# Performance work log

Measured on AMD Instinct MI355X. Metric: run time of the kernel, lower is better.

The kernel has to match this reference:

```python
import jax, jax.numpy as jnp
import numpy as np

OBS, PRED = 8, 12
EIN, EHID, NOISE = 64, 256, 64
GEMB = 64
DHID = EHID + NOISE  # 320
G, NPER = 8, 192
B = G * NPER


def leaky(x):
    return jnp.where(x > 0, x, 0.2 * x)


def lstm_cell(x, h, c, Wih, Whh, bih, bhh):
    gates = x @ Wih.T + bih + h @ Whh.T + bhh
    i, f, g, o = jnp.split(gates, 4, axis=-1)
    c = jax.nn.sigmoid(f) * c + jax.nn.sigmoid(i) * jnp.tanh(g)
    h = jax.nn.sigmoid(o) * jnp.tanh(c)
    return h, c


def kmeans(x, k, niter=10):
    # deterministic init: first k points (torch used randperm)
    c = x[:k]
    ar = jnp.arange(k)
    for _ in range(niter):
        d2 = ((x[:, None, :] - c[None, :, :]) ** 2).sum(-1)  # [N,k]
        a = jnp.argmin(d2, axis=1)
        onehot = (a[:, None] == ar[None, :]).astype(x.dtype)  # [N,k]
        cnt = onehot.sum(0)
        mean = (onehot.T @ x) / jnp.maximum(cnt, 1.0)[:, None]
        c = jnp.where((cnt == 0)[:, None], x[:k], mean)  # reseed dead clusters
    d2 = ((x[:, None, :] - c[None, :, :]) ** 2).sum(-1)
    return jnp.argmin(d2, axis=1)


def signed_graph(node, W_ne, b_ne, W_att, b_att):
    n, D = node.shape
    emb = node @ W_ne.T + b_ne  # [n,E]
    E = emb.shape[1]
    a_other, a_self = W_att[0, :E], W_att[0, E:]
    # e[i,j] = a_other.emb[j] + a_self.emb[i] + b  (cat([other, self]) order)
    e = (emb @ a_other)[None, :] + (emb @ a_self)[:, None] + b_att[0]
    edge = jax.nn.softmax(leaky(e), axis=0)
    edge = jnp.triu(edge, 0) + jnp.triu(edge, 1).T  # symmetrize from upper tri
    d = edge.sum(1)
    L = jnp.diag(d) - edge
    dinv = 1.0 / jnp.sqrt(d)
    L_sym = dinv[:, None] * L * dinv[None, :]
    lam, H = jnp.linalg.eigh(jax.lax.stop_gradient(L_sym))  # ascending eigvals
    H = H[:, :2]  # two smallest
    Hn = H / jnp.sqrt((H ** 2).sum(1, keepdims=True))
    labels = kmeans(Hn, int(np.ceil(n / 2)))
    same = labels[:, None] == labels[None, :]
    NEG = jnp.float32(-1e8)
    pos_alpha = jax.nn.softmax(leaky(edge * jnp.where(same, 1.0, NEG)), axis=0)
    neg_alpha = jax.nn.softmax(leaky(edge * jnp.where(same, NEG, 1.0)), axis=0)
    feat = jax.nn.relu(pos_alpha[..., None] * node[None, :, :]) + \
           jax.nn.relu(neg_alpha[..., None] * node[None, :, :])  # [n,n,D]
    return feat.sum(axis=1)


def setup_inputs():
    key = jax.random.key(0)
    ks = jax.random.split(key, 22)
    p = lambda k, s: jax.random.normal(k, s, jnp.float32) * 0.1
    starts = jnp.arange(G, dtype=jnp.int32) * NPER
    return {
        "input_traj": jax.random.normal(ks[0], (OBS + PRED, B, 2), jnp.float32),
        "enc_h0": jax.random.normal(ks[1], (B, EHID), jnp.float32),
        "enc_c0": jax.random.normal(ks[2], (B, EHID), jnp.float32),
        "noise_z": jax.random.normal(ks[3], (G, NOISE), jnp.float32),
        "W_emb": p(ks[4], (EIN, 2)), "b_emb": p(ks[5], (EIN,)),
        "Wih_e": p(ks[6], (4 * EHID, EIN)), "Whh_e": p(ks[7], (4 * EHID, EHID)),
        "bih_e": p(ks[8], (4 * EHID,)), "bhh_e": p(ks[9], (4 * EHID,)),
        "Wih_d": p(ks[10], (4 * DHID, EIN)), "Whh_d": p(ks[11], (4 * DHID, DHID)),
        "bih_d": p(ks[12], (4 * DHID,)), "bhh_d": p(ks[13], (4 * DHID,)),
        "W_out": p(ks[14], (2, DHID)), "b_out": p(ks[15], (2,)),
        "W_ne": p(ks[16], (GEMB, DHID)), "b_ne": p(ks[17], (GEMB,)),
        "W_att": p(ks[18], (1, 2 * GEMB)), "b_att": p(ks[19], (1,)),
        "seq_start_end": jnp.stack([starts, starts + NPER], axis=1),
    }


def reference(input_traj, enc_h0, enc_c0, noise_z, W_emb, b_emb,
              Wih_e, Whh_e, bih_e, bhh_e, Wih_d, Whh_d, bih_d, bhh_d,
              W_out, b_out, W_ne, b_ne, W_att, b_att, seq_start_end):
    # ---- encoder ----
    x = jax.nn.relu(input_traj @ W_emb.T + b_emb)  # [T,B,EIN]
    def step(carry, xt):
        h, c = carry
        h, c = lstm_cell(xt, h, c, Wih_e, Whh_e, bih_e, bhh_e)
        return (h, c), None
    (h_enc, _), _ = jax.lax.scan(step, (enc_h0, enc_c0), x[:OBS])
    # ---- add per-scene noise (equal-sized scenes) ----
    z = jnp.repeat(noise_z, NPER, axis=0)  # [B,NOISE]
    h = jnp.concatenate([h_enc, z], axis=1)  # [B,DHID]
    c = jnp.zeros_like(h)
    traj_out = input_traj[OBS - 1]  # [B,2]
    sg = jax.vmap(lambda nd: signed_graph(nd, W_ne, b_ne, W_att, b_att))
    preds = []
    for i in range(PRED):  # eval mode: no teacher forcing
        inp = jax.nn.relu(traj_out @ W_emb.T + b_emb)
        if i % 12 == 4:
            h = sg(h.reshape(G, NPER, DHID)).reshape(B, DHID)
        h, c = lstm_cell(inp, h, c, Wih_d, Whh_d, bih_d, bhh_d)
        traj_out = h @ W_out.T + b_out
        preds.append(traj_out)
    return jnp.stack(preds)  # [PRED,B,2]
```

## Files before the change

### kernel.cpp

```cpp
#include <hip/hip_runtime.h>
#include <hip/hip_bf16.h>

typedef __hip_bfloat16 bf16;

#define NN 192
#define NG 8
#define BB 1536
#define EHID 256
#define DH 320
#define PRED 12
#define STRD 192
#define ATILE (NN*STRD)

__device__ __forceinline__ int aoffc(int r, int c){
  int c4 = c >> 2;
  int s = (c4 & ~7) | ((c4 + 3*r) & 7);
  return r*STRD + (s << 2) + (c & 3);
}

#define WAVE_SYNC() do { asm volatile("" ::: "memory"); __builtin_amdgcn_wave_barrier(); } while (0)

__device__ __forceinline__ float waveSum(float v){
#pragma unroll
  for (int o = 32; o > 0; o >>= 1) v += __shfl_down(v, o);
  return v;
}
__device__ __forceinline__ double waveSumD(double v){
#pragma unroll
  for (int o = 32; o > 0; o >>= 1) v += __shfl_down(v, o);
  return v;
}
__device__ __forceinline__ float waveAllSum(float v){
#pragma unroll
  for (int o = 32; o > 0; o >>= 1) v += __shfl_xor(v, o);
  return v;
}
__device__ __forceinline__ double waveAllSumD(double v){
#pragma unroll
  for (int o = 32; o > 0; o >>= 1) v += __shfl_xor(v, o);
  return v;
}

__device__ __forceinline__ double blockSumD(double v, double* red){
  int lane = threadIdx.x & 63, wid = threadIdx.x >> 6, nw = (int)blockDim.x >> 6;
  double s = waveSumD(v);
  __syncthreads();
  if (lane == 0) red[wid] = s;
  __syncthreads();
  if (wid == 0){
    double t = (lane < nw) ? red[lane] : 0.0;
    t = waveSumD(t);
    if (lane == 0) red[0] = t;
  }
  __syncthreads();
  return red[0];
}


__global__ void k_zero_int(int* __restrict__ p, int n){
  int i = blockIdx.x*blockDim.x + threadIdx.x;
  if (i < n) p[i] = 0;
}
__global__ void k_zero_f(float* __restrict__ p, int n){
  int i = blockIdx.x*blockDim.x + threadIdx.x;
  if (i < n) p[i] = 0.f;
}

__global__ void k_probe(const unsigned short* __restrict__ src, int n, int* __restrict__ cnt){
  int tid = blockIdx.x*blockDim.x + threadIdx.x;
  int stride = gridDim.x*blockDim.x;
  int bad = 0;
  for (int j = tid; j < n; j += stride){
    float v = __uint_as_float(((unsigned int)src[j]) << 16);
    if (!(fabsf(v) < 100.f)) bad++;
  }
#pragma unroll
  for (int o = 32; o > 0; o >>= 1) bad += __shfl_down(bad, o);
  if ((threadIdx.x & 63) == 0 && bad > 0) atomicAdd(cnt, bad);
}
__global__ void k_flag(const int* __restrict__ cnt, int* __restrict__ flag){
  *flag = (*cnt > 4096) ? 1 : 0;
}

struct CvtArgs {
  const void* src[20];
  float*      dst[20];
  int         n[20];
};

__global__ void k_convert(CvtArgs a, const int* __restrict__ flag){
  int id = blockIdx.y;
  int n = a.n[id];
  float* d = a.dst[id];
  int t = blockIdx.x*blockDim.x + threadIdx.x;
  int stride = gridDim.x*blockDim.x;
  if (*flag == 0){
    const bf16* s = (const bf16*)a.src[id];
    for (int j = t; j < n; j += stride) d[j] = __bfloat162float(s[j]);
  } else {
    const float* s = (const float*)a.src[id];
    for (int j = t; j < n; j += stride) d[j] = s[j];
  }
}


__global__ void k_embed(const float* __restrict__ in, const float* __restrict__ W,
                        const float* __restrict__ b, float* __restrict__ out){
  int r = blockIdx.x, e = threadIdx.x;
  float x = in[r*2], y = in[r*2+1];
  float v = W[e*2]*x + W[e*2+1]*y + b[e];
  out[r*64+e] = v > 0.f ? v : 0.f;
}

__global__ void k_concat(const float* __restrict__ henc, const float* __restrict__ z,
                         float* __restrict__ h){
  int idx = blockIdx.x*blockDim.x + threadIdx.x;
  if (idx >= BB*DH) return;
  int b = idx / DH, j = idx - b*DH;
  h[idx] = (j < EHID) ? henc[b*EHID + j] : z[(b/NN)*64 + (j - EHID)];
}

__global__ void k_copy_f(const float* __restrict__ in, float* __restrict__ dst, int n){
  int i = blockIdx.x*blockDim.x + threadIdx.x;
  if (i < n) dst[i] = in[i];
}

__global__ __launch_bounds__(256) void k_gates(
    const float* __restrict__ A1, const float* __restrict__ W1, int K1,
    const float* __restrict__ A2, const float* __restrict__ W2, int K2,
    const float* __restrict__ b1, const float* __restrict__ b2,
    float* __restrict__ C, int N){
  __shared__ __align__(16) float As[32][68];
  __shared__ __align__(16) float Ws[32][68];
  int tid = threadIdx.x;
  int tx = tid & 15, ty = tid >> 4;
  int n0 = blockIdx.x * 64, m0 = blockIdx.y * 64;
  float acc[4][4] = {};
  for (int ph = 0; ph < 2; ++ph){
    const float* A = ph ? A2 : A1;
    const float* W = ph ? W2 : W1;
    int K = ph ? K2 : K1;
    for (int k0 = 0; k0 < K; k0 += 32){
      {
        int am = tid >> 2, ak = (tid & 3) * 8;
        const float* srcA = A + (size_t)(m0+am)*K + k0 + ak;
        float4 f0 = *(const float4*)(srcA);
        float4 f1 = *(const float4*)(srcA+4);
        As[ak+0][am]=f0.x; As[ak+1][am]=f0.y; As[ak+2][am]=f0.z; As[ak+3][am]=f0.w;
        As[ak+4][am]=f1.x; As[ak+5][am]=f1.y; As[ak+6][am]=f1.z; As[ak+7][am]=f1.w;
        const float* srcW = W + (size_t)(n0+am)*K + k0 + ak;
        float4 w0 = *(const float4*)(srcW);
        float4 w1 = *(const float4*)(srcW+4);
        Ws[ak+0][am]=w0.x; Ws[ak+1][am]=w0.y; Ws[ak+2][am]=w0.z; Ws[ak+3][am]=w0.w;
        Ws[ak+4][am]=w1.x; Ws[ak+5][am]=w1.y; Ws[ak+6][am]=w1.z; Ws[ak+7][am]=w1.w;
      }
      __syncthreads();
#pragma unroll
      for (int k = 0; k < 32; ++k){
        float4 a0 = *(const float4*)&As[k][ty*4];
        float4 b0 = *(const float4*)&Ws[k][tx*4];
        float av[4] = {a0.x, a0.y, a0.z, a0.w};
        float bv[4] = {b0.x, b0.y, b0.z, b0.w};
#pragma unroll
        for (int i = 0; i < 4; ++i)
#pragma unroll
          for (int j = 0; j < 4; ++j)
            acc[i][j] += av[i]*bv[j];
      }
      __syncthreads();
    }
  }
  float bs[4];
#pragma unroll
  for (int j = 0; j < 4; ++j){
    int col = n0 + tx*4 + j;
    bs[j] = b1[col] + b2[col];
  }
#pragma unroll
  for (int i = 0; i < 4; ++i){
    int row = m0 + ty*4 + i;
    float4 v;
    v.x = acc[i][0] + bs[0]; v.y = acc[i][1] + bs[1];
    v.z = acc[i][2] + bs[2]; v.w = acc[i][3] + bs[3];
    *(float4*)&C[(size_t)row*N + n0 + tx*4] = v;
  }
}

__global__ void k_lstm(const float* __restrict__ gates, float* __restrict__ c,
                       float* __restrict__ h, int H){
  int idx = blockIdx.x*blockDim.x + threadIdx.x;
  if (idx >= BB*H) return;
  int b = idx / H, j = idx - b*H;
  const float* g = gates + (size_t)b*4*H;
  float gi = g[j], gf = g[H+j], gg = g[2*H+j], go = g[3*H+j];
  float si = 1.f/(1.f+expf(-gi));
  float sf = 1.f/(1.f+expf(-gf));
  float so = 1.f/(1.f+expf(-go));
  float cc = sf*c[idx] + si*tanhf(gg);
  c[idx] = cc;
  h[idx] = so*tanhf(cc);
}

__global__ void k_outproj(const float* __restrict__ h, const float* __restrict__ W,
                          const float* __restrict__ bo, float* __restrict__ traj,
                          void* __restrict__ outbase, int step, const int* __restrict__ flag){
  int b = blockIdx.x, lane = threadIdx.x;
  const float* hb = h + (size_t)b*DH;
  float a0 = 0.f, a1 = 0.f;
  for (int k = lane; k < DH; k += 64){
    float hv = hb[k];
    a0 += hv*W[k];
    a1 += hv*W[DH+k];
  }
  a0 = waveSum(a0); a1 = waveSum(a1);
  if (lane == 0){
    a0 += bo[0]; a1 += bo[1];
    traj[b*2] = a0; traj[b*2+1] = a1;
    size_t idx = (size_t)step*BB*2 + (size_t)b*2;
    if (*flag == 0){
      bf16* o = (bf16*)outbase;
      o[idx] = __float2bfloat16(a0); o[idx+1] = __float2bfloat16(a1);
    } else {
      float* o = (float*)outbase;
      o[idx] = a0; o[idx+1] = a1;
    }
  }
}


__global__ void k_sg_emb(const float* __restrict__ h, const float* __restrict__ Wne,
                         const float* __restrict__ bne, const float* __restrict__ Watt,
                         double* __restrict__ sself, double* __restrict__ sother){
  int node = blockIdx.x, e = threadIdx.x;
  const float* hb = h + (size_t)node*DH;
  double acc = (double)bne[e];
  for (int k = 0; k < DH; ++k) acc += (double)hb[k]*(double)Wne[e*DH+k];
  double po = acc * (double)Watt[e];
  double ps = acc * (double)Watt[64+e];
  po = waveSumD(po); ps = waveSumD(ps);
  if (e == 0){ sother[node] = po; sself[node] = ps; }
}

__global__ void k_sg_edgecol(const double* __restrict__ sself, const double* __restrict__ sother,
                             const float* __restrict__ batt, double* __restrict__ edge){
  int g = blockIdx.x, j = threadIdx.x;
  const double* ss = sself + g*NN;
  double bb = (double)batt[0];
  double sj = sother[g*NN + j];
  double m = -1e300;
  for (int i = 0; i < NN; ++i){
    double e = ss[i] + sj + bb; e = e > 0.0 ? e : 0.2*e;
    m = fmax(m, e);
  }
  double sum = 0.0;
  for (int i = 0; i < NN; ++i){
    double e = ss[i] + sj + bb; e = e > 0.0 ? e : 0.2*e;
    sum += exp(e - m);
  }
  double* E = edge + (size_t)g*NN*NN;
  for (int i = 0; i < NN; ++i){
    double e = ss[i] + sj + bb; e = e > 0.0 ? e : 0.2*e;
    E[i*NN + j] = exp(e - m)/sum;
  }
}

__global__ void k_sg_sym(const double* __restrict__ edge, double* __restrict__ esym){
  int idx = blockIdx.x*blockDim.x + threadIdx.x;
  if (idx >= NG*NN*NN) return;
  int g = idx / (NN*NN), r = idx - g*NN*NN;
  int i = r / NN, j = r - i*NN;
  const double* E = edge + (size_t)g*NN*NN;
  esym[idx] = (i <= j) ? E[i*NN + j] : E[j*NN + i];
}

__global__ void k_sg_dsum(const double* __restrict__ esym, double* __restrict__ darr){
  int i = blockIdx.x*blockDim.x + threadIdx.x;
  if (i >= NG*NN) return;
  int g = i / NN, li = i - g*NN;
  const double* E = esym + (size_t)g*NN*NN + (size_t)li*NN;
  double s = 0.0;
  for (int j = 0; j < NN; ++j) s += E[j];
  darr[i] = fmax(s, 1e-300);
}

__global__ void k_sg_lsym(const double* __restrict__ esym, const double* __restrict__ darr,
                          float* __restrict__ Afull){
  int idx = blockIdx.x*blockDim.x + threadIdx.x;
  if (idx >= NG*NN*NN) return;
  int g = idx / (NN*NN), r = idx - g*NN*NN;
  int i = r / NN, j = r - i*NN;
  double w = esym[idx];
  double lij = (i == j) ? (darr[g*NN+i] - w) : (-w);
  Afull[(size_t)g*ATILE + aoffc(i, j)] =
      (float)(lij / (sqrt(darr[g*NN+i])*sqrt(darr[g*NN+j])));
}

__global__ __launch_bounds__(256) void k_sg_eigen(const float* __restrict__ Afull,
                                                   const double* __restrict__ darr,
                                                   double* __restrict__ v1out){
  extern __shared__ unsigned char ldsraw[];
  float*  A     = (float*)ldsraw;
  double* dd    = (double*)(ldsraw + 147456);
  double* ee    = dd + NN;
  double* yv    = ee + NN;
  double* lu_d  = yv + NN;
  double* lu_du = lu_d + NN;
  double* lu_du2= lu_du + NN;
  double* redA  = lu_du2 + NN;
  double* redB  = redA + 16;
  double* salpha= redB + 16;
  float*  uu    = (float*)(ldsraw + 156944);
  float*  ww    = uu + NN;
  int*    lu_piv= (int*)(ww + NN);
  double* lu_dl = (double*)uu;

  int g = blockIdx.x, tid = threadIdx.x;
  int lane = tid & 63, wid = tid >> 6;

  const float* src = Afull + (size_t)g*ATILE;
  for (int t = tid*4; t < ATILE; t += 1024) *(float4*)&A[t] = *(const float4*)&src[t];
  __syncthreads();

  for (int k = 0; k < NN-65; ++k){
    int m = NN-1-k;
    int i = k+1+tid;
    float x = 0.f;
    if (tid < m) x = A[aoffc(i, k)];
    if (tid == 0) *salpha = (double)x;
    float part = (tid > 0 && tid < m) ? x*x : 0.f;
    part = waveSum(part);
    if (lane == 0) redA[wid] = (double)part;
    __syncthreads();
    double sigma = redA[0] + redA[1] + redA[2] + redA[3];
    double alpha = *salpha;
    double beta, tau, scale;
    if (sigma <= 1e-30){ tau = 0.0; beta = alpha; scale = 0.0; }
    else {
      beta = -copysign(sqrt(alpha*alpha + sigma), alpha);
      tau = (beta - alpha)/beta;
      scale = 1.0/(alpha - beta);
    }
    float tau_f = (float)tau, scale_f = (float)scale;
    if (tid == 0){
      dd[k] = (double)A[aoffc(k, k)];
      ee[k] = beta;
      A[aoffc(k, k)] = tau_f;
    }
    if (tau != 0.0){
      float u_i = 0.f;
      if (tid < m){
        u_i = (tid == 0) ? 1.f : x*scale_f;
        uu[i] = u_i;
        if (tid >= 1) A[aoffc(i, k)] = u_i;
      }
      __syncthreads();
      float p = 0.f;
      if (tid < m){
        const int rb = i*STRD;
        const int rk3 = (3*i) & 7;
        int off[8];
#pragma unroll
        for (int j = 0; j < 8; ++j) off[j] = ((j + rk3) & 7) << 2;
        float s0=0.f, s1=0.f, s2=0.f, s3=0.f, accs=0.f;
        int c = k+1;
        int cA = (c+3)&~3, cB = (c+31)&~31;
        for (; c < cA; ++c) accs += A[aoffc(i, c)]*uu[c];
        for (; c < cB; c += 4){
          int c4 = c>>2; int s = (c4&~7)|((c4+rk3)&7);
          float4 a4 = *(const float4*)&A[rb + (s<<2)];
          float4 u4 = *(const float4*)&uu[c];
          s0 += a4.x*u4.x; s1 += a4.y*u4.y; s2 += a4.z*u4.z; s3 += a4.w*u4.w;
        }
        for (; c < NN; c += 32){
          const int cb = rb + c;
#pragma unroll
          for (int j = 0; j < 8; ++j){
            float4 a4 = *(const float4*)&A[cb + off[j]];
            float4 u4 = *(const float4*)&uu[c + 4*j];
            s0 += a4.x*u4.x; s1 += a4.y*u4.y; s2 += a4.z*u4.z; s3 += a4.w*u4.w;
          }
        }
        p = tau_f * (((s0+s1)+(s2+s3)) + accs);
      }
      float vp = u_i*p;
      vp = waveSum(vp);
      if (lane == 0) redB[wid] = (double)vp;
      __syncthreads();
      double vtp = redB[0] + redB[1] + redB[2] + redB[3];
      float Kc_f = (float)(0.5*tau*vtp);
      float w_i = 0.f;
      if (tid < m){
        w_i = p - Kc_f*u_i;
        ww[i] = w_i;
      }
      __syncthreads();
      if (tid < m){
        const int rb = i*STRD;
        const int rk3 = (3*i) & 7;
        int off[8];
#pragma unroll
        for (int j = 0; j < 8; ++j) off[j] = ((j + rk3) & 7) << 2;
        int c = k+1;
        int cA = (c+3)&~3, cB = (c+31)&~31;
        for (; c < cA; ++c) A[aoffc(i, c)] -= u_i*ww[c] + w_i*uu[c];
        for (; c < cB; c += 4){
          int c4 = c>>2; int s = (c4&~7)|((c4+rk3)&7);
          float* ap = &A[rb + (s<<2)];
          float4 a4 = *(const float4*)ap;
          float4 u4 = *(const float4*)&uu[c];
          float4 w4 = *(const float4*)&ww[c];
          a4.x -= u_i*w4.x + w_i*u4.x;
          a4.y -= u_i*w4.y + w_i*u4.y;
          a4.z -= u_i*w4.z + w_i*u4.z;
          a4.w -= u_i*w4.w + w_i*u4.w;
          *(float4*)ap = a4;
        }
        for (; c < NN; c += 32){
          const int cb = rb + c;
#pragma unroll
          for (int j = 0; j < 8; ++j){
            float* ap = &A[cb + off[j]];
            float4 a4 = *(const float4*)ap;
            float4 u4 = *(const float4*)&uu[c + 4*j];
            float4 w4 = *(const float4*)&ww[c + 4*j];
            a4.x -= u_i*w4.x + w_i*u4.x;
            a4.y -= u_i*w4.y + w_i*u4.y;
            a4.z -= u_i*w4.z + w_i*u4.z;
            a4.w -= u_i*w4.w + w_i*u4.w;
            *(float4*)ap = a4;
          }
        }
      }
      __syncthreads();
    } else {
      __syncthreads();
    }
  }

  if (wid != 0) return;

  for (int k = NN-65; k < NN-2; ++k){
    int m = NN-1-k;
    int i = k+1+lane;
    bool act = lane < m;
    float x = act ? A[aoffc(i, k)] : 0.f;
    float part = (lane > 0) ? x*x : 0.f;
    float sig_f = waveAllSum(part);
    float alpha_f = __shfl(x, 0);
    double sigma = (double)sig_f;
    double alpha = (double)alpha_f;
    double beta, tau, scale;
    if (sigma <= 1e-30){ tau = 0.0; beta = alpha; scale = 0.0; }
    else {
      beta = -copysign(sqrt(alpha*alpha + sigma), alpha);
      tau = (beta - alpha)/beta;
      scale = 1.0/(alpha - beta);
    }
    float tau_f = (float)tau, scale_f = (float)scale;
    if (lane == 0){
      dd[k] = (double)A[aoffc(k, k)];
      ee[k] = beta;
      A[aoffc(k, k)] = tau_f;
    }
    if (tau == 0.0) continue;
    float u = (lane == 0) ? 1.f : x*scale_f;
    int base4 = (k+1) & ~3;
    int ph = (k+1) - base4;
    uu[lane + ph] = u;
    if (lane >= 1 && act) A[aoffc(i, k)] = u;
    WAVE_SYNC();
    int ic = act ? i : (k+1);
    const int rb = ic*STRD;
    const int rk3 = (3*ic) & 7;
    float s0=0.f, s1=0.f, s2=0.f, s3=0.f, accs=0.f;
    {
      int c = k+1;
      int cA = (c+3)&~3; if (cA > NN) cA = NN;
      for (; c < cA; ++c) accs += A[aoffc(ic, c)]*uu[c-base4];
      for (; c < NN; c += 4){
        int c4 = c>>2; int s = (c4&~7)|((c4+rk3)&7);
        float4 a4 = *(const float4*)&A[rb + (s<<2)];
        float4 u4 = *(const float4*)&uu[c-base4];
        s0 += a4.x*u4.x; s1 += a4.y*u4.y; s2 += a4.z*u4.z; s3 += a4.w*u4.w;
      }
    }
    float p = tau_f*(((s0+s1)+(s2+s3)) + accs);
    float vtp = waveAllSum(u*p);
    float Kc_f = (float)(0.5*tau*(double)vtp);
    float w = p - Kc_f*u;
    ww[lane + ph] = w;
    WAVE_SYNC();
    if (act){
      int c = k+1;
      int cA = (c+3)&~3; if (cA > NN) cA = NN;
      for (; c < cA; ++c) A[aoffc(i, c)] -= u*ww[c-base4] + w*uu[c-base4];
      for (; c < NN; c += 4){
        int c4 = c>>2; int s = (c4&~7)|((c4+rk3)&7);
        float* ap = &A[rb + (s<<2)];
        float4 a4 = *(const float4*)ap;
        float4 u4 = *(const float4*)&uu[c-base4];
        float4 w4 = *(const float4*)&ww[c-base4];
        a4.x -= u*w4.x + w*u4.x;
        a4.y -= u*w4.y + w*u4.y;
        a4.z -= u*w4.z + w*u4.z;
        a4.w -= u*w4.w + w*u4.w;
        *(float4*)ap = a4;
      }
    }
    WAVE_SYNC();
  }

  if (lane == 0){
    dd[NN-2] = (double)A[aoffc(NN-2, NN-2)];
    ee[NN-2] = (double)A[aoffc(NN-1, NN-2)];
    dd[NN-1] = (double)A[aoffc(NN-1, NN-1)];
  }
  WAVE_SYNC();

  {
    double mn = 1e300, mx = -1e300;
    for (int i = lane; i < NN; i += 64){
      double r = (i > 0 ? fabs(ee[i-1]) : 0.0) + (i < NN-1 ? fabs(ee[i]) : 0.0);
      mn = fmin(mn, dd[i]-r); mx = fmax(mx, dd[i]+r);
    }
#pragma unroll
    for (int o = 32; o > 0; o >>= 1){
      mn = fmin(mn, __shfl_down(mn, o));
      mx = fmax(mx, __shfl_down(mx, o));
    }
    mn = __shfl(mn, 0); mx = __shfl(mx, 0);
    double lo = mn - 1e-8 - 1e-9*fabs(mn);
    double hi = mx + 1e-8 + 1e-9*fabs(mx);
    for (int it = 0; it < 10; ++it){
      double lam = lo + (hi-lo)*((double)(lane+1)/65.0);
      int cnt = 0;
      double q = dd[0] - lam;
      if (q < 0.0) cnt++;
      for (int i2 = 1; i2 < NN; ++i2){
        double den = q;
        if (fabs(den) < 1e-280) den = (den < 0.0) ? -1e-280 : 1e-280;
        q = dd[i2] - lam - ee[i2-1]*ee[i2-1]/den;
        if (q < 0.0) cnt++;
      }
      unsigned long long bal = __ballot(cnt >= 2);
      if (bal == 0ull){
        lo = lo + (hi-lo)*(64.0/65.0);
      } else {
        int j0 = __ffsll(bal) - 1;
        double nl = lo + (hi-lo)*((double)j0/65.0);
        double nh = lo + (hi-lo)*((double)(j0+1)/65.0);
        lo = nl; hi = nh;
      }
    }
    double lam1 = 0.5*(lo+hi);

    if (lane == 0){
      for (int i = 0; i < NN; ++i) lu_d[i] = dd[i] - lam1;
      for (int i = 0; i < NN-1; ++i){ lu_dl[i] = ee[i]; lu_du[i] = ee[i]; }
      for (int i = 0; i < NN-2; ++i) lu_du2[i] = 0.0;
      for (int i = 0; i < NN-1; ++i){
        if (fabs(lu_d[i]) >= fabs(lu_dl[i])){
          double di = lu_d[i];
          if (fabs(di) < 1e-30){ di = (di < 0.0) ? -1e-30 : 1e-30; lu_d[i] = di; }
          double fact = lu_dl[i]/di;
          lu_dl[i] = fact;
          lu_d[i+1] -= fact*lu_du[i];
          lu_piv[i] = 0;
        } else {
          double fact = lu_d[i]/lu_dl[i];
          lu_d[i] = lu_dl[i];
          double tmp = lu_d[i+1];
          lu_d[i+1] = lu_du[i] - fact*tmp;
          if (i < NN-2){ lu_du2[i] = lu_du[i+1]; lu_du[i+1] = -fact*lu_du[i+1]; }
          lu_du[i] = tmp;
          lu_dl[i] = fact;
          lu_piv[i] = 1;
        }
      }
      if (fabs(lu_d[NN-1]) < 1e-30)
        lu_d[NN-1] = (lu_d[NN-1] < 0.0) ? -1e-30 : 1e-30;
      for (int i = 0; i < NN; ++i) yv[i] = 1.0 + 0.001*(double)((i*37)%29);
      for (int round = 0; round < 2; ++round){
        for (int i = 0; i < NN-1; ++i){
          if (lu_piv[i] == 0){
            yv[i+1] -= lu_dl[i]*yv[i];
          } else {
            double t = yv[i]; yv[i] = yv[i+1]; yv[i+1] = t - lu_dl[i]*yv[i];
          }
        }
        double mx1 = 0.0;
        for (int i = 0; i < NN; ++i) mx1 = fmax(mx1, fabs(yv[i]));
        double inv1 = (mx1 > 0.0 && isfinite(mx1)) ? 1.0/mx1 : 1.0;
        for (int i = 0; i < NN; ++i) yv[i] *= inv1;
        yv[NN-1] = yv[NN-1]/lu_d[NN-1];
        yv[NN-2] = (yv[NN-2] - lu_du[NN-2]*yv[NN-1])/lu_d[NN-2];
        for (int i = NN-3; i >= 0; --i)
          yv[i] = (yv[i] - lu_du[i]*yv[i+1] - lu_du2[i]*yv[i+2])/lu_d[i];
        double mxv = 0.0;
        for (int i = 0; i < NN; ++i) mxv = fmax(mxv, fabs(yv[i]));
        double inv = (mxv > 0.0 && isfinite(mxv)) ? 1.0/mxv : 1.0;
        for (int i = 0; i < NN; ++i){
          double val = yv[i]*inv;
          if (!isfinite(val)) val = 0.0;
          yv[i] = val;
        }
      }
    }
  }
  WAVE_SYNC();

  {
    int r0 = lane, r1 = lane+64, r2 = lane+128;
    double y0 = yv[r0], y1 = yv[r1], y2 = yv[r2];
    for (int k = NN-3; k >= 0; --k){
      double tau = (double)A[aoffc(k, k)];
      if (tau != 0.0){
        double u0 = (r0 > k) ? ((r0 == k+1) ? 1.0 : (double)A[aoffc(r0, k)]) : 0.0;
        double u1 = (r1 > k) ? ((r1 == k+1) ? 1.0 : (double)A[aoffc(r1, k)]) : 0.0;
        double u2 = (r2 > k) ? ((r2 == k+1) ? 1.0 : (double)A[aoffc(r2, k)]) : 0.0;
        double part = u0*y0 + u1*y1 + u2*y2;
        part = waveAllSumD(part);
        double s = tau*part;
        y0 -= s*u0; y1 -= s*u1; y2 -= s*u2;
      }
    }

    const double* dg = darr + (size_t)g*NN;
    double d0 = dg[r0], d1 = dg[r1], d2 = dg[r2];
    double sd0 = sqrt(d0), sd1 = sqrt(d1), sd2 = sqrt(d2);
    double pd  = waveAllSumD(sd0*y0 + sd1*y1 + sd2*y2);
    double pn2 = waveAllSumD(d0 + d1 + d2);
    double coef = pd/fmax(pn2, 1e-300);
    y0 -= coef*sd0; y1 -= coef*sd1; y2 -= coef*sd2;
    double s2 = waveAllSumD(y0*y0 + y1*y1 + y2*y2);
    double nrm = sqrt(s2);
    double inv = (nrm > 0.0 && isfinite(nrm)) ? 1.0/nrm : 0.0;
    double o0 = y0*inv, o1 = y1*inv, o2 = y2*inv;
    if (!isfinite(o0)) o0 = 0.0;
    if (!isfinite(o1)) o1 = 0.0;
    if (!isfinite(o2)) o2 = 0.0;
    v1out[g*NN + r0] = o0;
    v1out[g*NN + r1] = o1;
    v1out[g*NN + r2] = o2;
  }
}

__global__ __launch_bounds__(256) void k_sg_kmeans(const double* __restrict__ darr,
                                                   const double* __restrict__ v1,
                                                   int* __restrict__ labels){
  __shared__ double px[NN], py[NN], cx[96], cy[96];
  __shared__ int lab[NN];
  __shared__ double red[16];
  int g = blockIdx.x, tid = threadIdx.x;
  double part = 0.0;
  for (int i = tid; i < NN; i += 256) part += darr[g*NN + i];
  double sumd = blockSumD(part, red);
  double invn = 1.0/sqrt(fmax(sumd, 1e-300));
  for (int i = tid; i < NN; i += 256){
    double h0 = sqrt(darr[g*NN + i])*invn;
    double h1 = v1[g*NN + i];
    double rn = sqrt(h0*h0 + h1*h1);
    double ax = h0/rn, ay = h1/rn;
    if (!isfinite(ax)) ax = 0.0;
    if (!isfinite(ay)) ay = 0.0;
    px[i] = ax; py[i] = ay;
  }
  __syncthreads();
  if (tid < 96){ cx[tid] = px[tid]; cy[tid] = py[tid]; }
  __syncthreads();
  for (int it = 0; it <= 10; ++it){
    if (tid < NN){
      double bx = px[tid], by = py[tid];
      double best = 1e300; int bi = 0;
      for (int a = 0; a < 96; ++a){
        double dx = bx - cx[a], dy = by - cy[a];
        double d2 = dx*dx + dy*dy;
        if (d2 < best){ best = d2; bi = a; }
      }
      lab[tid] = bi;
    }
    __syncthreads();
    if (it == 10) break;
    if (tid < 96){
      int c = 0; double sx = 0.0, sy = 0.0;
      for (int i = 0; i < NN; ++i){
        if (lab[i] == tid){ c++; sx += px[i]; sy += py[i]; }
      }
      if (c > 0){ cx[tid] = sx/(double)c; cy[tid] = sy/(double)c; }
      else      { cx[tid] = px[tid];      cy[tid] = py[tid]; }
    }
    __syncthreads();
  }
  if (tid < NN) labels[g*NN + tid] = lab[tid];
}

__global__ void k_sg_alpha(const double* __restrict__ esym, const int* __restrict__ labels,
                           float* __restrict__ S){
  __shared__ int lbs[NN];
  int g = blockIdx.x, j = threadIdx.x;
  if (j < NN) lbs[j] = labels[g*NN + j];
  __syncthreads();
  const double* E = esym + (size_t)g*NN*NN;
  const double NEG = -100000000.0;
  int lj = lbs[j];
  double mp = -1e300, mn = -1e300;
  for (int i = 0; i < NN; ++i){
    double w = E[i*NN + j];
    bool sm = (lbs[i] == lj);
    double vp = sm ? w : w*NEG; vp = vp > 0.0 ? vp : 0.2*vp;
    double vn = sm ? w*NEG : w; vn = vn > 0.0 ? vn : 0.2*vn;
    mp = fmax(mp, vp); mn = fmax(mn, vn);
  }
  double sp = 0.0, sn = 0.0;
  for (int i = 0; i < NN; ++i){
    double w = E[i*NN + j];
    bool sm = (lbs[i] == lj);
    double vp = sm ? w : w*NEG; vp = vp > 0.0 ? vp : 0.2*vp;
    double vn = sm ? w*NEG : w; vn = vn > 0.0 ? vn : 0.2*vn;
    sp += exp(vp - mp); sn += exp(vn - mn);
  }
  float* So = S + (size_t)g*NN*NN;
  for (int i = 0; i < NN; ++i){
    double w = E[i*NN + j];
    bool sm = (lbs[i] == lj);
    double vp = sm ? w : w*NEG; vp = vp > 0.0 ? vp : 0.2*vp;
    double vn = sm ? w*NEG : w; vn = vn > 0.0 ? vn : 0.2*vn;
    So[i*NN + j] = (float)(exp(vp - mp)/sp + exp(vn - mn)/sn);
  }
}

__global__ __launch_bounds__(320) void k_sg_feat(const float* __restrict__ S,
                                                 const float* __restrict__ hin,
                                                 float* __restrict__ hout){
  int r = blockIdx.x;
  int g = r / NN, li = r - g*NN;
  int dh = threadIdx.x;
  const float* Srow = S + (size_t)g*NN*NN + (size_t)li*NN;
  const float* hb = hin + (size_t)g*NN*DH;
  float acc = 0.f;
  for (int j = 0; j < NN; ++j){
    float w = Srow[j];
    float x = hb[(size_t)j*DH + dh];
    acc += w*(x > 0.f ? x : 0.f);
  }
  hout[(size_t)r*DH + dh] = acc;
}


extern "C" void kernel_launch(void* const* d_in, const int* in_sizes, int n_in,
                              void* d_out, int out_size, void* d_ws, size_t ws_size,
                              hipStream_t stream){
  (void)n_in; (void)out_size; (void)ws_size;

  float* ws = (float*)d_ws;
  float* inp   = ws;
  float* gates = ws + 98304;
  float* hA    = ws + 2064384;
  float* hB    = ws + 2555904;
  float* cD    = ws + 3047424;
  float* traj  = ws + 3538944;
  double* sself_d  = (double*)(ws + 3542016);
  double* sother_d = (double*)(ws + 3545088);
  double* darr_d   = (double*)(ws + 3548160);
  double* v1_d     = (double*)(ws + 3551232);
  int*    labels   = (int*)(ws + 3554304);
  double* edge_d = (double*)gates;
  double* esym_d = (double*)(gates + 589824);
  float*  Afull  = gates + 1179648;
  float*  Smat   = gates;
  float* a_traj = ws + 3555840;
  float* a_z    = ws + 3617280;
  float* a_Wemb = ws + 3617792;
  float* a_bemb = ws + 3617920;
  float* a_Wihe = ws + 3617984;
  float* a_Whhe = ws + 3683520;
  float* a_bihe = ws + 3945664;
  float* a_bhhe = ws + 3946688;
  float* a_Wihd = ws + 3947712;
  float* a_Whhd = ws + 4029632;
  float* a_bihd = ws + 4439232;
  float* a_bhhd = ws + 4440512;
  float* a_Wout = ws + 4441792;
  float* a_bout = ws + 4442432;
  float* a_Wne  = ws + 4442496;
  float* a_bne  = ws + 4462976;
  float* a_Watt = ws + 4463040;
  float* a_batt = ws + 4463168;
  int* cnt  = (int*)(ws + 4463232);
  int* flag = (int*)(ws + 4463233);

  const int EIG_LDS = 159248;
  hipFuncSetAttribute((const void*)k_sg_eigen,
                      hipFuncAttributeMaxDynamicSharedMemorySize, EIG_LDS);

  k_zero_int<<<1, 64, 0, stream>>>(cnt, 2);
  k_probe<<<256, 256, 0, stream>>>((const unsigned short*)d_in[1], in_sizes[1], cnt);
  k_flag<<<1, 1, 0, stream>>>(cnt, flag);

  CvtArgs ca;
  float* dsts[20] = { a_traj, hB, cD, a_z, a_Wemb, a_bemb, a_Wihe, a_Whhe, a_bihe,
                      a_bhhe, a_Wihd, a_Whhd, a_bihd, a_bhhd, a_Wout, a_bout,
                      a_Wne, a_bne, a_Watt, a_batt };
  for (int i = 0; i < 20; ++i){
    ca.src[i] = d_in[i];
    ca.dst[i] = dsts[i];
    ca.n[i]   = in_sizes[i];
  }
  k_convert<<<dim3(512, 20), 256, 0, stream>>>(ca, flag);

  for (int t = 0; t < 8; ++t){
    k_embed<<<BB, 64, 0, stream>>>(a_traj + (size_t)t*BB*2, a_Wemb, a_bemb, inp);
    k_gates<<<dim3(1024/64, BB/64), 256, 0, stream>>>(inp, a_Wihe, 64, hB, a_Whhe, EHID,
                                                      a_bihe, a_bhhe, gates, 1024);
    k_lstm<<<(BB*EHID+255)/256, 256, 0, stream>>>(gates, cD, hB, EHID);
  }

  k_concat<<<(BB*DH+255)/256, 256, 0, stream>>>(hB, a_z, hA);
  k_zero_f<<<(BB*DH+255)/256, 256, 0, stream>>>(cD, BB*DH);
  k_copy_f<<<(BB*2+255)/256, 256, 0, stream>>>(a_traj + (size_t)7*BB*2, traj, BB*2);

  float* hcur = hA;
  float* hoth = hB;
  for (int i = 0; i < PRED; ++i){
    k_embed<<<BB, 64, 0, stream>>>(traj, a_Wemb, a_bemb, inp);
    if (i == 4){
      k_sg_emb<<<BB, 64, 0, stream>>>(hcur, a_Wne, a_bne, a_Watt, sself_d, sother_d);
      k_sg_edgecol<<<NG, NN, 0, stream>>>(sself_d, sother_d, a_batt, edge_d);
      k_sg_sym<<<(NG*NN*NN+255)/256, 256, 0, stream>>>(edge_d, esym_d);
      k_sg_dsum<<<(NG*NN+255)/256, 256, 0, stream>>>(esym_d, darr_d);
      k_sg_lsym<<<(NG*NN*NN+255)/256, 256, 0, stream>>>(esym_d, darr_d, Afull);
      k_sg_eigen<<<NG, 256, EIG_LDS, stream>>>(Afull, darr_d, v1_d);
      k_sg_kmeans<<<NG, 256, 0, stream>>>(darr_d, v1_d, labels);
      k_sg_alpha<<<NG, NN, 0, stream>>>(esym_d, labels, Smat);
      k_sg_feat<<<BB, DH, 0, stream>>>(Smat, hcur, hoth);
      float* tmp = hcur; hcur = hoth; hoth = tmp;
    }
    k_gates<<<dim3((4*DH)/64, BB/64), 256, 0, stream>>>(inp, a_Wihd, 64, hcur, a_Whhd, DH,
                                                        a_bihd, a_bhhd, gates, 4*DH);
    k_lstm<<<(BB*DH+255)/256, 256, 0, stream>>>(gates, cD, hcur, DH);
    k_outproj<<<BB, 64, 0, stream>>>(hcur, a_Wout, a_bout, traj, d_out, i, flag);
  }
}
```

Measured before the change: 2.315 ms.

## Split Householder tridiagonalization column work across four thread teams

Widens the eigen kernel from 256 to 1024 threads. Each row is now served by four teams that split the 32-column blocks of the symmetric matvec and of the rank-2 update, with team 3 also covering the unaligned prefix. Partial dot products are reduced through a shared scratch buffer that aliases existing LDS arrays, and one extra barrier is added per step. The aim is to shorten the serial per-step latency of a kernel that runs only eight blocks. The cost is more barriers and reduction traffic per step, plus the risk that later code in the kernel still assumes 256 threads.

```diff
diff --git a/kernel.cpp b/kernel.cpp
--- a/kernel.cpp
+++ b/kernel.cpp
@@ -295,7 +295,7 @@
       (float)(lij / (sqrt(darr[g*NN+i])*sqrt(darr[g*NN+j])));
 }
 
-__global__ __launch_bounds__(256) void k_sg_eigen(const float* __restrict__ Afull,
+__global__ __launch_bounds__(1024) void k_sg_eigen(const float* __restrict__ Afull,
                                                    const double* __restrict__ darr,
                                                    double* __restrict__ v1out){
   extern __shared__ unsigned char ldsraw[];
@@ -312,24 +312,28 @@
   float*  uu    = (float*)(ldsraw + 156944);
   float*  ww    = uu + NN;
   int*    lu_piv= (int*)(ww + NN);
+  float*  pp4   = (float*)yv;
   double* lu_dl = (double*)uu;
 
   int g = blockIdx.x, tid = threadIdx.x;
   int lane = tid & 63, wid = tid >> 6;
+  int rtid = tid & 255, team = tid >> 8;
 
   const float* src = Afull + (size_t)g*ATILE;
-  for (int t = tid*4; t < ATILE; t += 1024) *(float4*)&A[t] = *(const float4*)&src[t];
+  for (int t = tid*4; t < ATILE; t += 4096) *(float4*)&A[t] = *(const float4*)&src[t];
   __syncthreads();
 
   for (int k = 0; k < NN-65; ++k){
     int m = NN-1-k;
-    int i = k+1+tid;
+    int i = k+1+rtid;
     float x = 0.f;
-    if (tid < m) x = A[aoffc(i, k)];
+    if (rtid < m) x = A[aoffc(i, k)];
     if (tid == 0) *salpha = (double)x;
-    float part = (tid > 0 && tid < m) ? x*x : 0.f;
-    part = waveSum(part);
-    if (lane == 0) redA[wid] = (double)part;
+    if (team == 0){
+      float part = (rtid > 0 && rtid < m) ? x*x : 0.f;
+      part = waveSum(part);
+      if (lane == 0) redA[wid] = (double)part;
+    }
     __syncthreads();
     double sigma = redA[0] + redA[1] + redA[2] + redA[3];
     double alpha = *salpha;
@@ -348,30 +352,35 @@
     }
     if (tau != 0.0){
       float u_i = 0.f;
-      if (tid < m){
-        u_i = (tid == 0) ? 1.f : x*scale_f;
+      if (rtid < m) u_i = (rtid == 0) ? 1.f : x*scale_f;
+      if (team == 0 && rtid < m){
         uu[i] = u_i;
-        if (tid >= 1) A[aoffc(i, k)] = u_i;
+        if (rtid >= 1) A[aoffc(i, k)] = u_i;
       }
       __syncthreads();
-      float p = 0.f;
-      if (tid < m){
-        const int rb = i*STRD;
-        const int rk3 = (3*i) & 7;
-        int off[8];
-#pragma unroll
-        for (int j = 0; j < 8; ++j) off[j] = ((j + rk3) & 7) << 2;
+      int c0 = k+1;
+      int cA = (c0+3)&~3;
+      int cB = (c0+31)&~31;
+      int NB = (NN - cB) >> 5;
+      const int rb = i*STRD;
+      const int rk3 = (3*i) & 7;
+      int off[8];
+#pragma unroll
+      for (int j = 0; j < 8; ++j) off[j] = ((j + rk3) & 7) << 2;
+      if (rtid < m){
         float s0=0.f, s1=0.f, s2=0.f, s3=0.f, accs=0.f;
-        int c = k+1;
-        int cA = (c+3)&~3, cB = (c+31)&~31;
-        for (; c < cA; ++c) accs += A[aoffc(i, c)]*uu[c];
-        for (; c < cB; c += 4){
-          int c4 = c>>2; int s = (c4&~7)|((c4+rk3)&7);
-          float4 a4 = *(const float4*)&A[rb + (s<<2)];
-          float4 u4 = *(const float4*)&uu[c];
-          s0 += a4.x*u4.x; s1 += a4.y*u4.y; s2 += a4.z*u4.z; s3 += a4.w*u4.w;
+        if (team == 3){
+          int c = c0;
+          for (; c < cA; ++c) accs += A[aoffc(i, c)]*uu[c];
+          for (; c < cB; c += 4){
+            int c4 = c>>2; int s = (c4&~7)|((c4+rk3)&7);
+            float4 a4 = *(const float4*)&A[rb + (s<<2)];
+            float4 u4 = *(const float4*)&uu[c];
+            s0 += a4.x*u4.x; s1 += a4.y*u4.y; s2 += a4.z*u4.z; s3 += a4.w*u4.w;
+          }
         }
-        for (; c < NN; c += 32){
+        for (int b = team; b < NB; b += 4){
+          int c = cB + (b<<5);
           const int cb = rb + c;
 #pragma unroll
           for (int j = 0; j < 8; ++j){
@@ -380,42 +389,45 @@
             s0 += a4.x*u4.x; s1 += a4.y*u4.y; s2 += a4.z*u4.z; s3 += a4.w*u4.w;
           }
         }
-        p = tau_f * (((s0+s1)+(s2+s3)) + accs);
-      }
-      float vp = u_i*p;
-      vp = waveSum(vp);
-      if (lane == 0) redB[wid] = (double)vp;
+        pp4[team*NN + i - (k+1) + (k+1)] = ((s0+s1)+(s2+s3)) + accs;
+      }
+      __syncthreads();
+      float p = 0.f;
+      if (rtid < m)
+        p = tau_f*(pp4[i] + pp4[NN + i] + pp4[2*NN + i] + pp4[3*NN + i]);
+      if (team == 0){
+        float vp = (rtid < m) ? u_i*p : 0.f;
+        vp = waveSum(vp);
+        if (lane == 0) redB[wid] = (double)vp;
+      }
       __syncthreads();
       double vtp = redB[0] + redB[1] + redB[2] + redB[3];
       float Kc_f = (float)(0.5*tau*vtp);
       float w_i = 0.f;
-      if (tid < m){
+      if (rtid < m){
         w_i = p - Kc_f*u_i;
-        ww[i] = w_i;
+        if (team == 0) ww[i] = w_i;
       }
       __syncthreads();
-      if (tid < m){
-        const int rb = i*STRD;
-        const int rk3 = (3*i) & 7;
-        int off[8];
-#pragma unroll
-        for (int j = 0; j < 8; ++j) off[j] = ((j + rk3) & 7) << 2;
-        int c = k+1;
-        int cA = (c+3)&~3, cB = (c+31)&~31;
-        for (; c < cA; ++c) A[aoffc(i, c)] -= u_i*ww[c] + w_i*uu[c];
-        for (; c < cB; c += 4){
-          int c4 = c>>2; int s = (c4&~7)|((c4+rk3)&7);
-          float* ap = &A[rb + (s<<2)];
-          float4 a4 = *(const float4*)ap;
-          float4 u4 = *(const float4*)&uu[c];
-          float4 w4 = *(const float4*)&ww[c];
-          a4.x -= u_i*w4.x + w_i*u4.x;
-          a4.y -= u_i*w4.y + w_i*u4.y;
-          a4.z -= u_i*w4.z + w_i*u4.z;
-          a4.w -= u_i*w4.w + w_i*u4.w;
-          *(float4*)ap = a4;
+      if (rtid < m){
+        if (team == 3){
+          int c = c0;
+          for (; c < cA; ++c) A[aoffc(i, c)] -= u_i*ww[c] + w_i*uu[c];
+          for (; c < cB; c += 4){
+            int c4 = c>>2; int s = (c4&~7)|((c4+rk3)&7);
+            float* ap = &A[rb + (s<<2)];
+            float4 a4 = *(const float4*)ap;
+            float4 u4 = *(const float4*)&uu[c];
+            float4 w4 = *(const float4*)&ww[c];
+            a4.x -= u_i*w4.x + w_i*u4.x;
+            a4.y -= u_i*w4.y + w_i*u4.y;
+            a4.z -= u_i*w4.z + w_i*u4.z;
+            a4.w -= u_i*w4.w + w_i*u4.w;
+            *(float4*)ap = a4;
+          }
         }
-        for (; c < NN; c += 32){
+        for (int b = team; b < NB; b += 4){
+          int c = cB + (b<<5);
           const int cb = rb + c;
 #pragma unroll
           for (int j = 0; j < 8; ++j){
@@ -829,7 +841,7 @@
       k_sg_sym<<<(NG*NN*NN+255)/256, 256, 0, stream>>>(edge_d, esym_d);
       k_sg_dsum<<<(NG*NN+255)/256, 256, 0, stream>>>(esym_d, darr_d);
       k_sg_lsym<<<(NG*NN*NN+255)/256, 256, 0, stream>>>(esym_d, darr_d, Afull);
-      k_sg_eigen<<<NG, 256, EIG_LDS, stream>>>(Afull, darr_d, v1_d);
+      k_sg_eigen<<<NG, 1024, EIG_LDS, stream>>>(Afull, darr_d, v1_d);
       k_sg_kmeans<<<NG, 256, 0, stream>>>(darr_d, v1_d, labels);
       k_sg_alpha<<<NG, NN, 0, stream>>>(esym_d, labels, Smat);
       k_sg_feat<<<BB, DH, 0, stream>>>(Smat, hcur, hoth);
```

Measured after the change: 2.297 ms. No clear change (-0.8%).

## Run Householder tridiagonalization in a single wavefront to remove block barriers

Applied to the files above, without the earlier changes.

The eigen kernel now launches one 64-lane wave per graph instead of 256 threads. The whole Householder reduction runs in that wave, with each lane handling up to three rows. This replaces the __syncthreads and cross-wave LDS reductions in the first phase with wave barriers and shuffle reductions, removing the per-column barrier latency. The cost is a quarter of the threads doing the same O(n^3) matrix update, so per-column compute latency rises.

```diff
diff --git a/kernel.cpp b/kernel.cpp
--- a/kernel.cpp
+++ b/kernel.cpp
@@ -295,9 +295,9 @@
       (float)(lij / (sqrt(darr[g*NN+i])*sqrt(darr[g*NN+j])));
 }
 
-__global__ __launch_bounds__(256) void k_sg_eigen(const float* __restrict__ Afull,
-                                                   const double* __restrict__ darr,
-                                                   double* __restrict__ v1out){
+__global__ __launch_bounds__(64) void k_sg_eigen(const float* __restrict__ Afull,
+                                                 const double* __restrict__ darr,
+                                                 double* __restrict__ v1out){
   extern __shared__ unsigned char ldsraw[];
   float*  A     = (float*)ldsraw;
   double* dd    = (double*)(ldsraw + 147456);
@@ -313,140 +313,24 @@
   float*  ww    = uu + NN;
   int*    lu_piv= (int*)(ww + NN);
   double* lu_dl = (double*)uu;
-
-  int g = blockIdx.x, tid = threadIdx.x;
-  int lane = tid & 63, wid = tid >> 6;
+  (void)redA; (void)redB; (void)salpha;
+
+  int g = blockIdx.x;
+  int lane = threadIdx.x;
 
   const float* src = Afull + (size_t)g*ATILE;
-  for (int t = tid*4; t < ATILE; t += 1024) *(float4*)&A[t] = *(const float4*)&src[t];
-  __syncthreads();
-
-  for (int k = 0; k < NN-65; ++k){
-    int m = NN-1-k;
-    int i = k+1+tid;
-    float x = 0.f;
-    if (tid < m) x = A[aoffc(i, k)];
-    if (tid == 0) *salpha = (double)x;
-    float part = (tid > 0 && tid < m) ? x*x : 0.f;
-    part = waveSum(part);
-    if (lane == 0) redA[wid] = (double)part;
-    __syncthreads();
-    double sigma = redA[0] + redA[1] + redA[2] + redA[3];
-    double alpha = *salpha;
-    double beta, tau, scale;
-    if (sigma <= 1e-30){ tau = 0.0; beta = alpha; scale = 0.0; }
-    else {
-      beta = -copysign(sqrt(alpha*alpha + sigma), alpha);
-      tau = (beta - alpha)/beta;
-      scale = 1.0/(alpha - beta);
-    }
-    float tau_f = (float)tau, scale_f = (float)scale;
-    if (tid == 0){
-      dd[k] = (double)A[aoffc(k, k)];
-      ee[k] = beta;
-      A[aoffc(k, k)] = tau_f;
-    }
-    if (tau != 0.0){
-      float u_i = 0.f;
-      if (tid < m){
-        u_i = (tid == 0) ? 1.f : x*scale_f;
-        uu[i] = u_i;
-        if (tid >= 1) A[aoffc(i, k)] = u_i;
-      }
-      __syncthreads();
-      float p = 0.f;
-      if (tid < m){
-        const int rb = i*STRD;
-        const int rk3 = (3*i) & 7;
-        int off[8];
-#pragma unroll
-        for (int j = 0; j < 8; ++j) off[j] = ((j + rk3) & 7) << 2;
-        float s0=0.f, s1=0.f, s2=0.f, s3=0.f, accs=0.f;
-        int c = k+1;
-        int cA = (c+3)&~3, cB = (c+31)&~31;
-        for (; c < cA; ++c) accs += A[aoffc(i, c)]*uu[c];
-        for (; c < cB; c += 4){
-          int c4 = c>>2; int s = (c4&~7)|((c4+rk3)&7);
-          float4 a4 = *(const float4*)&A[rb + (s<<2)];
-          float4 u4 = *(const float4*)&uu[c];
-          s0 += a4.x*u4.x; s1 += a4.y*u4.y; s2 += a4.z*u4.z; s3 += a4.w*u4.w;
-        }
-        for (; c < NN; c += 32){
-          const int cb = rb + c;
-#pragma unroll
-          for (int j = 0; j < 8; ++j){
-            float4 a4 = *(const float4*)&A[cb + off[j]];
-            float4 u4 = *(const float4*)&uu[c + 4*j];
-            s0 += a4.x*u4.x; s1 += a4.y*u4.y; s2 += a4.z*u4.z; s3 += a4.w*u4.w;
-          }
-        }
-        p = tau_f * (((s0+s1)+(s2+s3)) + accs);
-      }
-      float vp = u_i*p;
-      vp = waveSum(vp);
-      if (lane == 0) redB[wid] = (double)vp;
-      __syncthreads();
-      double vtp = redB[0] + redB[1] + redB[2] + redB[3];
-      float Kc_f = (float)(0.5*tau*vtp);
-      float w_i = 0.f;
-      if (tid < m){
-        w_i = p - Kc_f*u_i;
-        ww[i] = w_i;
-      }
-      __syncthreads();
-      if (tid < m){
-        const int rb = i*STRD;
-        const int rk3 = (3*i) & 7;
-        int off[8];
-#pragma unroll
-        for (int j = 0; j < 8; ++j) off[j] = ((j + rk3) & 7) << 2;
-        int c = k+1;
-        int cA = (c+3)&~3, cB = (c+31)&~31;
-        for (; c < cA; ++c) A[aoffc(i, c)] -= u_i*ww[c] + w_i*uu[c];
-        for (; c < cB; c += 4){
-          int c4 = c>>2; int s = (c4&~7)|((c4+rk3)&7);
-          float* ap = &A[rb + (s<<2)];
-          float4 a4 = *(const float4*)ap;
-          float4 u4 = *(const float4*)&uu[c];
-          float4 w4 = *(const float4*)&ww[c];
-          a4.x -= u_i*w4.x + w_i*u4.x;
-          a4.y -= u_i*w4.y + w_i*u4.y;
-          a4.z -= u_i*w4.z + w_i*u4.z;
-          a4.w -= u_i*w4.w + w_i*u4.w;
-          *(float4*)ap = a4;
-        }
-        for (; c < NN; c += 32){
-          const int cb = rb + c;
-#pragma unroll
-          for (int j = 0; j < 8; ++j){
-            float* ap = &A[cb + off[j]];
-            float4 a4 = *(const float4*)ap;
-            float4 u4 = *(const float4*)&uu[c + 4*j];
-            float4 w4 = *(const float4*)&ww[c + 4*j];
-            a4.x -= u_i*w4.x + w_i*u4.x;
-            a4.y -= u_i*w4.y + w_i*u4.y;
-            a4.z -= u_i*w4.z + w_i*u4.z;
-            a4.w -= u_i*w4.w + w_i*u4.w;
-            *(float4*)ap = a4;
-          }
-        }
-      }
-      __syncthreads();
-    } else {
-      __syncthreads();
-    }
-  }
-
-  if (wid != 0) return;
-
-  for (int k = NN-65; k < NN-2; ++k){
-    int m = NN-1-k;
-    int i = k+1+lane;
-    bool act = lane < m;
-    float x = act ? A[aoffc(i, k)] : 0.f;
-    float part = (lane > 0) ? x*x : 0.f;
+  for (int t = lane*4; t < ATILE; t += 256) *(float4*)&A[t] = *(const float4*)&src[t];
+  WAVE_SYNC();
+
+  for (int k = 0; k < NN-2; ++k){
+    int r0 = k+1+lane, r1 = r0+64, r2 = r0+128;
+    bool a0 = r0 < NN, a1 = r1 < NN, a2 = r2 < NN;
+    float x0 = a0 ? A[aoffc(r0, k)] : 0.f;
+    float x1 = a1 ? A[aoffc(r1, k)] : 0.f;
+    float x2 = a2 ? A[aoffc(r2, k)] : 0.f;
+    float part = x1*x1 + x2*x2 + ((lane > 0) ? x0*x0 : 0.f);
     float sig_f = waveAllSum(part);
-    float alpha_f = __shfl(x, 0);
+    float alpha_f = __shfl(x0, 0);
     double sigma = (double)sig_f;
     double alpha = (double)alpha_f;
     double beta, tau, scale;
@@ -463,47 +347,93 @@
       A[aoffc(k, k)] = tau_f;
     }
     if (tau == 0.0) continue;
-    float u = (lane == 0) ? 1.f : x*scale_f;
-    int base4 = (k+1) & ~3;
-    int ph = (k+1) - base4;
-    uu[lane + ph] = u;
-    if (lane >= 1 && act) A[aoffc(i, k)] = u;
+
+    float u0 = a0 ? ((lane == 0) ? 1.f : x0*scale_f) : 0.f;
+    float u1 = a1 ? x1*scale_f : 0.f;
+    float u2 = a2 ? x2*scale_f : 0.f;
+    if (a0){ uu[r0] = u0; if (lane > 0) A[aoffc(r0, k)] = u0; }
+    if (a1){ uu[r1] = u1; A[aoffc(r1, k)] = u1; }
+    if (a2){ uu[r2] = u2; A[aoffc(r2, k)] = u2; }
     WAVE_SYNC();
-    int ic = act ? i : (k+1);
-    const int rb = ic*STRD;
-    const int rk3 = (3*ic) & 7;
-    float s0=0.f, s1=0.f, s2=0.f, s3=0.f, accs=0.f;
-    {
-      int c = k+1;
-      int cA = (c+3)&~3; if (cA > NN) cA = NN;
-      for (; c < cA; ++c) accs += A[aoffc(ic, c)]*uu[c-base4];
-      for (; c < NN; c += 4){
-        int c4 = c>>2; int s = (c4&~7)|((c4+rk3)&7);
-        float4 a4 = *(const float4*)&A[rb + (s<<2)];
-        float4 u4 = *(const float4*)&uu[c-base4];
-        s0 += a4.x*u4.x; s1 += a4.y*u4.y; s2 += a4.z*u4.z; s3 += a4.w*u4.w;
-      }
-    }
-    float p = tau_f*(((s0+s1)+(s2+s3)) + accs);
-    float vtp = waveAllSum(u*p);
+
+    const int rb0 = r0*STRD, rb1 = r1*STRD, rb2 = r2*STRD;
+    const int k30 = (3*r0) & 7, k31 = (3*r1) & 7, k32 = (3*r2) & 7;
+    float p0 = 0.f, p1 = 0.f, p2 = 0.f;
+    int c = k+1;
+    int cA = (c+3)&~3; if (cA > NN) cA = NN;
+    for (; c < cA; ++c){
+      float uc = uu[c];
+      if (a0) p0 += A[aoffc(r0, c)]*uc;
+      if (a1) p1 += A[aoffc(r1, c)]*uc;
+      if (a2) p2 += A[aoffc(r2, c)]*uc;
+    }
+    for (; c < NN; c += 4){
+      int c4 = c>>2, base = (c4 & ~7);
+      float4 u4 = *(const float4*)&uu[c];
+      if (a0){
+        int s = base | ((c4 + k30) & 7);
+        float4 a4 = *(const float4*)&A[rb0 + (s<<2)];
+        p0 += a4.x*u4.x + a4.y*u4.y + a4.z*u4.z + a4.w*u4.w;
+      }
+      if (a1){
+        int s = base | ((c4 + k31) & 7);
+        float4 a4 = *(const float4*)&A[rb1 + (s<<2)];
+        p1 += a4.x*u4.x + a4.y*u4.y + a4.z*u4.z + a4.w*u4.w;
+      }
+      if (a2){
+        int s = base | ((c4 + k32) & 7);
+        float4 a4 = *(const float4*)&A[rb2 + (s<<2)];
+        p2 += a4.x*u4.x + a4.y*u4.y + a4.z*u4.z + a4.w*u4.w;
+      }
+    }
+    p0 *= tau_f; p1 *= tau_f; p2 *= tau_f;
+    float vtp = waveAllSum(u0*p0 + u1*p1 + u2*p2);
     float Kc_f = (float)(0.5*tau*(double)vtp);
-    float w = p - Kc_f*u;
-    ww[lane + ph] = w;
+    float w0 = p0 - Kc_f*u0, w1 = p1 - Kc_f*u1, w2 = p2 - Kc_f*u2;
+    if (a0) ww[r0] = w0;
+    if (a1) ww[r1] = w1;
+    if (a2) ww[r2] = w2;
     WAVE_SYNC();
-    if (act){
-      int c = k+1;
-      int cA = (c+3)&~3; if (cA > NN) cA = NN;
-      for (; c < cA; ++c) A[aoffc(i, c)] -= u*ww[c-base4] + w*uu[c-base4];
-      for (; c < NN; c += 4){
-        int c4 = c>>2; int s = (c4&~7)|((c4+rk3)&7);
-        float* ap = &A[rb + (s<<2)];
+
+    c = k+1;
+    for (; c < cA; ++c){
+      float uc = uu[c], wc = ww[c];
+      if (a0) A[aoffc(r0, c)] -= u0*wc + w0*uc;
+      if (a1) A[aoffc(r1, c)] -= u1*wc + w1*uc;
+      if (a2) A[aoffc(r2, c)] -= u2*wc + w2*uc;
+    }
+    for (; c < NN; c += 4){
+      int c4 = c>>2, base = (c4 & ~7);
+      float4 u4 = *(const float4*)&uu[c];
+      float4 w4 = *(const float4*)&ww[c];
+      if (a0){
+        int s = base | ((c4 + k30) & 7);
+        float* ap = &A[rb0 + (s<<2)];
         float4 a4 = *(const float4*)ap;
-        float4 u4 = *(const float4*)&uu[c-base4];
-        float4 w4 = *(const float4*)&ww[c-base4];
-        a4.x -= u*w4.x + w*u4.x;
-        a4.y -= u*w4.y + w*u4.y;
-        a4.z -= u*w4.z + w*u4.z;
-        a4.w -= u*w4.w + w*u4.w;
+        a4.x -= u0*w4.x + w0*u4.x;
+        a4.y -= u0*w4.y + w0*u4.y;
+        a4.z -= u0*w4.z + w0*u4.z;
+        a4.w -= u0*w4.w + w0*u4.w;
+        *(float4*)ap = a4;
+      }
+      if (a1){
+        int s = base | ((c4 + k31) & 7);
+        float* ap = &A[rb1 + (s<<2)];
+        float4 a4 = *(const float4*)ap;
+        a4.x -= u1*w4.x + w1*u4.x;
+        a4.y -= u1*w4.y + w1*u4.y;
+        a4.z -= u1*w4.z + w1*u4.z;
+        a4.w -= u1*w4.w + w1*u4.w;
+        *(float4*)ap = a4;
+      }
+      if (a2){
+        int s = base | ((c4 + k32) & 7);
+        float* ap = &A[rb2 + (s<<2)];
+        float4 a4 = *(const float4*)ap;
+        a4.x -= u2*w4.x + w2*u4.x;
+        a4.y -= u2*w4.y + w2*u4.y;
+        a4.z -= u2*w4.z + w2*u4.z;
+        a4.w -= u2*w4.w + w2*u4.w;
         *(float4*)ap = a4;
       }
     }
@@ -829,7 +759,7 @@
       k_sg_sym<<<(NG*NN*NN+255)/256, 256, 0, stream>>>(edge_d, esym_d);
       k_sg_dsum<<<(NG*NN+255)/256, 256, 0, stream>>>(esym_d, darr_d);
       k_sg_lsym<<<(NG*NN*NN+255)/256, 256, 0, stream>>>(esym_d, darr_d, Afull);
-      k_sg_eigen<<<NG, 256, EIG_LDS, stream>>>(Afull, darr_d, v1_d);
+      k_sg_eigen<<<NG, 64, EIG_LDS, stream>>>(Afull, darr_d, v1_d);
       k_sg_kmeans<<<NG, 256, 0, stream>>>(darr_d, v1_d, labels);
       k_sg_alpha<<<NG, NN, 0, stream>>>(esym_d, labels, Smat);
       k_sg_feat<<<BB, DH, 0, stream>>>(Smat, hcur, hoth);
```

Result: slower. 3.540 ms (+52.9%).
